# Performance work log

Hardware: AMD Instinct MI355X
Metric: run time of the kernel (lower is better)

The kernel has to match this reference:

```python
import jax, jax.numpy as jnp
import numpy as np

B, D, H = 128, 256, 512  # batch, input_size, hidden_size; 2 hidden layers
ORDER = 'A'
EPS = 1e-12


def _masks():
    # Standard MADE sequential degrees: inputs 1..D (reversed for order 'B'),
    # hidden degrees cycle over 1..D-1. Hidden mask: >=, output mask: > (strict).
    din = np.arange(1, D + 1) if ORDER == 'A' else np.arange(D, 0, -1)
    dh = (np.arange(H) % (D - 1)) + 1
    m0 = (dh[:, None] >= din[None, :]).astype(np.float32)  # [H, D]
    m1 = (dh[:, None] >= dh[None, :]).astype(np.float32)   # [H, H]
    mo = (din[:, None] > dh[None, :]).astype(np.float32)   # [D, H]
    return jnp.asarray(m0), jnp.asarray(m1), jnp.asarray(mo)


def _made(y, W0, b0, W1, b1, Wo, bo, masks):
    m0, m1, mo = masks
    h = jax.nn.elu(y @ (W0 * m0).T + b0)   # [B, H]
    h = jax.nn.elu(h @ (W1 * m1).T + b1)   # [B, H]
    return h @ (Wo * mo).T + bo            # [B, D]


def setup_inputs() -> dict:
    key = jax.random.key(0)
    ks = jax.random.split(key, 13)
    s_in, s_h = 1.0 / np.sqrt(D), 1.0 / np.sqrt(H)

    def p(k, shape, s):
        return (jax.random.normal(k, shape, jnp.float32) * s).astype(jnp.float32)

    return {
        'x': jax.random.normal(ks[0], (B, D), jnp.float32),
        'mu_W0': p(ks[1], (H, D), s_in), 'mu_b0': jnp.zeros((H,), jnp.float32),
        'mu_W1': p(ks[2], (H, H), s_h),  'mu_b1': jnp.zeros((H,), jnp.float32),
        'mu_Wo': p(ks[3], (D, H), s_h),  'mu_bo': jnp.zeros((D,), jnp.float32),
        'lv_W0': p(ks[4], (H, D), s_in), 'lv_b0': jnp.zeros((H,), jnp.float32),
        'lv_W1': p(ks[5], (H, H), s_h),  'lv_b1': jnp.zeros((H,), jnp.float32),
        'lv_Wo': p(ks[6], (D, H), s_h),  'lv_bo': jnp.zeros((D,), jnp.float32),
    }


def reference(x, mu_W0, mu_b0, mu_W1, mu_b1, mu_Wo, mu_bo,
              lv_W0, lv_b0, lv_W1, lv_b1, lv_Wo, lv_bo):
    masks = _masks()
    idx = jnp.arange(D) if ORDER == 'A' else jnp.arange(D - 1, -1, -1)

    def step(carry, i):
        y, _ = carry
        mu = _made(y, mu_W0, mu_b0, mu_W1, mu_b1, mu_Wo, mu_bo, masks)
        logstd = 0.5 * _made(y, lv_W0, lv_b0, lv_W1, lv_b1, lv_Wo, lv_bo, masks)
        new_col = (x[:, i] - mu[:, i]) / (jnp.exp(logstd[:, i]) + EPS)
        y = y.at[:, i].set(new_col)
        return (y, logstd), None

    init = (jnp.zeros_like(x), jnp.zeros_like(x))
    (y, logstd), _ = jax.lax.scan(step, init, idx)
    return y, logstd.sum(axis=1)
```

## Files before the change

### kernel.cpp

```cpp
#include <hip/hip_runtime.h>

#define DD 256
#define HH 512
#define BB 128
#define TS 4096

#define WAITVM(N) asm volatile("s_waitcnt vmcnt(" #N ")" ::: "memory")
#define PIN4(v) asm volatile("" :: "v"((v).x), "v"((v).y), "v"((v).z), "v"((v).w))

__device__ __forceinline__ float elu_f(float x) {
    return x > 0.f ? x : (__expf(x) - 1.f);
}
__device__ __forceinline__ float rlf(float v, int l) {
    return __uint_as_float(__builtin_amdgcn_readlane(__float_as_uint(v), (unsigned)l));
}
__device__ __forceinline__ float f4c(const float4& v, int r) {
    return r == 0 ? v.x : r == 1 ? v.y : r == 2 ? v.z : v.w;
}

__device__ __forceinline__ int pmap(int h) {
    if (h == 510) return 255;
    if (h == 511) return 511;
    return (h < 255) ? (4 * (h & 63) + (h >> 6))
                     : (256 + 4 * ((h - 255) & 63) + ((h - 255) >> 6));
}
__device__ __forceinline__ int p4map(int j) {
    return 4 * (j & 63) + (j >> 6);
}
__device__ __forceinline__ int w1base(int hp) {
    return (hp <= 254) ? hp * TS
         : (hp <= 509) ? (hp - 255) * TS + 1024
         : 255 * TS + ((hp == 510) ? 0 : 1024);
}
__device__ __forceinline__ int wobase(int hp) {
    return (hp <= 254) ? hp * TS + 3072
         : (hp <= 509) ? (hp - 255) * TS + 3584
         : 255 * TS + ((hp == 510) ? 2048 : 2560);
}

__global__ __launch_bounds__(256) void prep(
    const float* __restrict__ w0m_, const float* __restrict__ w0l_,
    const float* __restrict__ w1m_, const float* __restrict__ w1l_,
    const float* __restrict__ wom_, const float* __restrict__ wol_,
    float* __restrict__ tape)
{
    __shared__ float tm[32][33], tl[32][33];
    const int tx = threadIdx.x & 31, ty = threadIdx.x >> 5;
    const unsigned b = blockIdx.x;

    if (b < 256) {
        const int h0 = (int)(b >> 4) << 5, hp0 = (int)(b & 15) << 5;
        #pragma unroll
        for (int j = 0; j < 4; ++j) {
            int r = ty + 8 * j;
            tm[r][tx] = w1m_[(h0 + r) * HH + hp0 + tx];
            tl[r][tx] = w1l_[(h0 + r) * HH + hp0 + tx];
        }
        __syncthreads();
        #pragma unroll
        for (int j = 0; j < 4; ++j) {
            int hp = hp0 + ty + 8 * j;
            int h  = h0 + tx;
            int dh_h = (h <= 254) ? h + 1 : (h <= 509 ? h - 254 : h - 509);
            int dh_p = (hp <= 254) ? hp + 1 : (hp <= 509 ? hp - 254 : hp - 509);
            float mask = (dh_h >= dh_p) ? 1.f : 0.f;
            int base = w1base(hp), p = pmap(h);
            tape[base + p]       = mask * tm[tx][ty + 8 * j];
            tape[base + 512 + p] = mask * tl[tx][ty + 8 * j];
        }
    } else if (b < 384) {
        const int b2 = (int)b - 256;
        const int h0 = (b2 >> 3) << 5, i0 = (b2 & 7) << 5;
        #pragma unroll
        for (int j = 0; j < 4; ++j) {
            int r = ty + 8 * j;
            tm[r][tx] = w0m_[(h0 + r) * DD + i0 + tx];
            tl[r][tx] = w0l_[(h0 + r) * DD + i0 + tx];
        }
        __syncthreads();
        #pragma unroll
        for (int j = 0; j < 4; ++j) {
            int i = i0 + ty + 8 * j;
            int h = h0 + tx;
            int p = pmap(h);
            tape[i * TS + 2048 + p] = tm[tx][ty + 8 * j];
            tape[i * TS + 2560 + p] = tl[tx][ty + 8 * j];
        }
    } else {
        const int b3 = (int)b - 384;
        const int j0 = (b3 >> 4) << 5, hp0 = (b3 & 15) << 5;
        #pragma unroll
        for (int j = 0; j < 4; ++j) {
            int r = ty + 8 * j;
            tm[r][tx] = wom_[(j0 + r) * HH + hp0 + tx];
            tl[r][tx] = wol_[(j0 + r) * HH + hp0 + tx];
        }
        __syncthreads();
        #pragma unroll
        for (int j = 0; j < 4; ++j) {
            int hp = hp0 + ty + 8 * j;
            int jj = j0 + tx;
            int base = wobase(hp), p = p4map(jj);
            tape[base + p]       = tm[tx][ty + 8 * j];
            tape[base + 256 + p] = tl[tx][ty + 8 * j];
        }
    }
}

__device__ __forceinline__ void stage16(const float* g, float* l, int lane) {
    #pragma unroll
    for (int k = 0; k < 16; ++k) {
        __builtin_amdgcn_global_load_lds(
            (const __attribute__((address_space(1))) void*)(g + 256 * k + 4 * lane),
            (__attribute__((address_space(3))) void*)(l + 256 * k),
            16, 0, 0);
    }
}

struct WSet { float4 w[16]; };

__device__ __forceinline__ void rdW(WSet& S, const float* b, int lane) {
    const float4* p = (const float4*)b;
    S.w[8]  = p[64 * 8 + lane];  S.w[9]  = p[64 * 9 + lane];
    S.w[10] = p[64 * 10 + lane]; S.w[11] = p[64 * 11 + lane];
    S.w[0]  = p[64 * 0 + lane];  S.w[4]  = p[64 * 4 + lane];
    S.w[1]  = p[64 * 1 + lane];  S.w[5]  = p[64 * 5 + lane];
    S.w[2]  = p[64 * 2 + lane];  S.w[6]  = p[64 * 6 + lane];
    S.w[3]  = p[64 * 3 + lane];  S.w[7]  = p[64 * 7 + lane];
    S.w[12] = p[64 * 12 + lane]; S.w[14] = p[64 * 14 + lane];
    S.w[13] = p[64 * 13 + lane]; S.w[15] = p[64 * 15 + lane];
}
__device__ __forceinline__ void pinW(const WSet& S) {
    #pragma unroll
    for (int k = 0; k < 16; ++k) PIN4(S.w[k]);
}

template<int Q, int EX>
__device__ __forceinline__ void stepF(
    int tl, int lane, float v, const WSet& S,
    float (&a0m)[8], float (&a0l)[8], float (&a1m)[8], float (&a1l)[8],
    float (&Rm)[4], float (&Rl)[4], float (&yv)[4],
    const float4& exmA, const float4& exmB, const float4& exlA, const float4& exlB,
    const float4& exwm, const float4& exwl)
{
    yv[Q] = (lane == tl) ? v : yv[Q];

    #pragma unroll
    for (int r = Q; r < 4; ++r) {
        a0m[r]     += v * f4c(S.w[8], r);
        a0m[4 + r] += v * f4c(S.w[9], r);
        a0l[r]     += v * f4c(S.w[10], r);
        a0l[4 + r] += v * f4c(S.w[11], r);
    }

    float p0m = elu_f(rlf(a0m[Q], tl)),     p0l = elu_f(rlf(a0l[Q], tl));
    float p1m = elu_f(rlf(a0m[4 + Q], tl)), p1l = elu_f(rlf(a0l[4 + Q], tl));
    float p2m = 0.f, p2l = 0.f;
    if (EX) {
        p2m = elu_f(rlf(a0m[EX == 1 ? 3 : 7], 63));
        p2l = elu_f(rlf(a0l[EX == 1 ? 3 : 7], 63));
    }

    #pragma unroll
    for (int r = Q; r < 4; ++r) {
        a1m[r]     += f4c(S.w[0], r) * p0m + f4c(S.w[4], r) * p1m;
        a1m[4 + r] += f4c(S.w[1], r) * p0m + f4c(S.w[5], r) * p1m;
        a1l[r]     += f4c(S.w[2], r) * p0l + f4c(S.w[6], r) * p1l;
        a1l[4 + r] += f4c(S.w[3], r) * p0l + f4c(S.w[7], r) * p1l;
    }
    if (EX) {
        #pragma unroll
        for (int r = 0; r < 4; ++r) {
            a1m[r]     += f4c(exmA, r) * p2m;
            a1m[4 + r] += f4c(exmB, r) * p2m;
            a1l[r]     += f4c(exlA, r) * p2l;
            a1l[4 + r] += f4c(exlB, r) * p2l;
        }
    }

    float q0m = elu_f(rlf(a1m[Q], tl)),     q0l = elu_f(rlf(a1l[Q], tl));
    float q1m = elu_f(rlf(a1m[4 + Q], tl)), q1l = elu_f(rlf(a1l[4 + Q], tl));
    float q2m = 0.f, q2l = 0.f;
    if (EX) {
        q2m = elu_f(rlf(a1m[EX == 1 ? 3 : 7], 63));
        q2l = elu_f(rlf(a1l[EX == 1 ? 3 : 7], 63));
    }

    #pragma unroll
    for (int r = Q; r < 4; ++r) {
        Rm[r] += f4c(S.w[12], r) * q0m + f4c(S.w[14], r) * q1m;
        Rl[r] += f4c(S.w[13], r) * q0l + f4c(S.w[15], r) * q1l;
    }
    if (EX) {
        #pragma unroll
        for (int r = 0; r < 4; ++r) {
            Rm[r] += f4c(exwm, r) * q2m;
            Rl[r] += f4c(exwl, r) * q2l;
        }
    }
}

__global__ __launch_bounds__(128, 1) void made_main(
    const float* __restrict__ x,
    const float* __restrict__ mu_b0, const float* __restrict__ mu_b1,
    const float* __restrict__ mu_bo,
    const float* __restrict__ lv_b0, const float* __restrict__ lv_b1,
    const float* __restrict__ lv_bo,
    const float* __restrict__ tape,
    float* __restrict__ out)
{
    __shared__ __align__(16) float buf[4][TS];
    const int row  = blockIdx.x;
    const int lane = threadIdx.x & 63;
    const int wid  = threadIdx.x >> 6;

    const float4 d4 = make_float4(0.f, 0.f, 0.f, 0.f);

    if (wid == 1) {
        #pragma unroll
        for (int g = 0; g < 3; ++g)
            stage16(tape + (size_t)g * TS, &buf[g][0], lane);
        #pragma unroll 1
        for (int t = 0; t < 255; ++t) {
            if (t < 253) { WAITVM(16); } else { WAITVM(0); }
            __builtin_amdgcn_s_barrier();
            __builtin_amdgcn_sched_barrier(0);
            int g = t + 3;
            if (g < 255)
                stage16(tape + (size_t)g * TS, &buf[g & 3][0], lane);
        }
        return;
    }

    float a0m[8], a0l[8], a1m[8], a1l[8], Rm[4], Rl[4], yv[4];
    float xv[4], bmv[4], blv[4];
    #pragma unroll
    for (int r = 0; r < 4; ++r) {
        a0m[r]     = mu_b0[lane + 64 * r];
        a0m[4 + r] = mu_b0[255 + lane + 64 * r];
        a0l[r]     = lv_b0[lane + 64 * r];
        a0l[4 + r] = lv_b0[255 + lane + 64 * r];
        a1m[r]     = mu_b1[lane + 64 * r];
        a1m[4 + r] = mu_b1[255 + lane + 64 * r];
        a1l[r]     = lv_b1[lane + 64 * r];
        a1l[4 + r] = lv_b1[255 + lane + 64 * r];
        Rm[r] = 0.f; Rl[r] = 0.f; yv[r] = 0.f;
        xv[r]  = x[row * DD + 64 * r + lane];
        bmv[r] = mu_bo[64 * r + lane];
        blv[r] = lv_bo[64 * r + lane];
    }
    if (lane == 63) {
        a0m[3] = mu_b0[510]; a0m[7] = mu_b0[511];
        a0l[3] = lv_b0[510]; a0l[7] = lv_b0[511];
        a1m[3] = mu_b1[510]; a1m[7] = mu_b1[511];
        a1l[3] = lv_b1[510]; a1l[7] = lv_b1[511];
    }

    const float4* a4 = (const float4*)(tape + 255 * TS);
    float4 e510mA = a4[lane],       e510mB = a4[64 + lane];
    float4 e510lA = a4[128 + lane], e510lB = a4[192 + lane];
    float4 e511mA = a4[256 + lane], e511mB = a4[320 + lane];
    float4 e511lA = a4[384 + lane], e511lB = a4[448 + lane];
    float4 wo510m = a4[512 + lane], wo510l = a4[576 + lane];
    float4 wo511m = a4[640 + lane], wo511l = a4[704 + lane];

    float ls_part = 0.f;
    float vloc;
    {
        float d0  = xv[0] - (Rm[0] + bmv[0]);
        float ls0 = 0.5f * (Rl[0] + blv[0]);
        float s0  = __fdividef(1.f, __expf(ls0) + 1e-12f);
        ls_part += (lane == 0) ? ls0 : 0.f;
        vloc = d0 * s0;
    }

    WSet W;

    __syncthreads();
    rdW(W, &buf[0][0], lane);
    {
        float v = rlf(vloc, 0);
        stepF<0, 1>(0, lane, v, W, a0m, a0l, a1m, a1l, Rm, Rl, yv,
                    e510mA, e510mB, e510lA, e510lB, wo510m, wo510l);
        rdW(W, &buf[1][0], lane);
        float d_  = xv[0] - (Rm[0] + bmv[0]);
        float ls_ = 0.5f * (Rl[0] + blv[0]);
        float s_  = __fdividef(1.f, __expf(ls_) + 1e-12f);
        ls_part += (lane == 1) ? ls_ : 0.f;
        vloc = d_ * s_;
        pinW(W);
    }

    __syncthreads();
    {
        float v = rlf(vloc, 1);
        stepF<0, 2>(1, lane, v, W, a0m, a0l, a1m, a1l, Rm, Rl, yv,
                    e511mA, e511mB, e511lA, e511lB, wo511m, wo511l);
        rdW(W, &buf[2][0], lane);
        float d_  = xv[0] - (Rm[0] + bmv[0]);
        float ls_ = 0.5f * (Rl[0] + blv[0]);
        float s_  = __fdividef(1.f, __expf(ls_) + 1e-12f);
        ls_part += (lane == 2) ? ls_ : 0.f;
        vloc = d_ * s_;
        pinW(W);
    }

#define FBODY(Q, tt, Qn, tn, PREF)                                            \
    {                                                                         \
        __syncthreads();                                                      \
        float v_ = rlf(vloc, (tt) & 63);                                      \
        stepF<Q, 0>((tt) & 63, lane, v_, W, a0m, a0l, a1m, a1l, Rm, Rl, yv,   \
                    d4, d4, d4, d4, d4, d4);                                  \
        if (PREF) rdW(W, &buf[((tt) + 1) & 3][0], lane);                      \
        float dn_  = xv[Qn] - (Rm[Qn] + bmv[Qn]);                             \
        float lsn_ = 0.5f * (Rl[Qn] + blv[Qn]);                               \
        float sn_  = __fdividef(1.f, __expf(lsn_) + 1e-12f);                  \
        ls_part += (lane == (tn)) ? lsn_ : 0.f;                               \
        vloc = dn_ * sn_;                                                     \
        if (PREF) pinW(W);                                                    \
    }

    #pragma unroll 1
    for (int t = 2; t < 63; ++t)    FBODY(0, t, 0, t + 1, 1)
    FBODY(0, 63, 1, 0, 1)
    #pragma unroll 1
    for (int t = 64; t < 127; ++t)  FBODY(1, t, 1, t - 63, 1)
    FBODY(1, 127, 2, 0, 1)
    #pragma unroll 1
    for (int t = 128; t < 191; ++t) FBODY(2, t, 2, t - 127, 1)
    FBODY(2, 191, 3, 0, 1)
    #pragma unroll 1
    for (int t = 192; t < 254; ++t) FBODY(3, t, 3, t - 191, 1)
    FBODY(3, 254, 3, 63, 0)
#undef FBODY

    yv[3] = (lane == 63) ? vloc : yv[3];

    #pragma unroll
    for (int r = 0; r < 4; ++r) out[row * DD + 64 * r + lane] = yv[r];

    #pragma unroll
    for (int off = 32; off; off >>= 1)
        ls_part += __shfl_down(ls_part, off);
    if (lane == 0) out[BB * DD + row] = ls_part;
}

extern "C" void kernel_launch(void* const* d_in, const int* in_sizes, int n_in,
                              void* d_out, int out_size, void* d_ws, size_t ws_size,
                              hipStream_t stream) {
    const float* x     = (const float*)d_in[0];
    const float* mu_W0 = (const float*)d_in[1];
    const float* mu_b0 = (const float*)d_in[2];
    const float* mu_W1 = (const float*)d_in[3];
    const float* mu_b1 = (const float*)d_in[4];
    const float* mu_Wo = (const float*)d_in[5];
    const float* mu_bo = (const float*)d_in[6];
    const float* lv_W0 = (const float*)d_in[7];
    const float* lv_b0 = (const float*)d_in[8];
    const float* lv_W1 = (const float*)d_in[9];
    const float* lv_b1 = (const float*)d_in[10];
    const float* lv_Wo = (const float*)d_in[11];
    const float* lv_bo = (const float*)d_in[12];

    float* tape = (float*)d_ws;

    prep<<<512, 256, 0, stream>>>(mu_W0, lv_W0, mu_W1, lv_W1, mu_Wo, lv_Wo, tape);
    made_main<<<BB, 128, 0, stream>>>(x, mu_b0, mu_b1, mu_bo,
                                      lv_b0, lv_b1, lv_bo, tape, (float*)d_out);
}
```

Measured before the change: 178.4 us.

## Batch tape staging into groups of four steps with an eight-slot LDS ring

The producer wave now stages four tape slices at a time into an 8-deep LDS ring and syncs with the compute wave once per four steps instead of every step. The compute wave drops the software prefetch and register pinning, loading each step's weights from LDS right before use. This is meant to cut per-step barrier overhead. In exchange it doubles LDS use to 128 KB and exposes LDS load latency on each step, since the next step's weights are no longer prefetched.

```diff
diff --git a/kernel.cpp b/kernel.cpp
--- a/kernel.cpp
+++ b/kernel.cpp
@@ -6,7 +6,7 @@
 #define TS 4096
 
 #define WAITVM(N) asm volatile("s_waitcnt vmcnt(" #N ")" ::: "memory")
-#define PIN4(v) asm volatile("" :: "v"((v).x), "v"((v).y), "v"((v).z), "v"((v).w))
+#define SBAR() do { __builtin_amdgcn_s_barrier(); __builtin_amdgcn_sched_barrier(0); } while (0)
 
 __device__ __forceinline__ float elu_f(float x) {
     return x > 0.f ? x : (__expf(x) - 1.f);
@@ -130,10 +130,6 @@
     S.w[12] = p[64 * 12 + lane]; S.w[14] = p[64 * 14 + lane];
     S.w[13] = p[64 * 13 + lane]; S.w[15] = p[64 * 15 + lane];
 }
-__device__ __forceinline__ void pinW(const WSet& S) {
-    #pragma unroll
-    for (int k = 0; k < 16; ++k) PIN4(S.w[k]);
-}
 
 template<int Q, int EX>
 __device__ __forceinline__ void stepF(
@@ -209,7 +205,7 @@
     const float* __restrict__ tape,
     float* __restrict__ out)
 {
-    __shared__ __align__(16) float buf[4][TS];
+    __shared__ __align__(16) float buf[8][TS];
     const int row  = blockIdx.x;
     const int lane = threadIdx.x & 63;
     const int wid  = threadIdx.x >> 6;
@@ -218,16 +214,21 @@
 
     if (wid == 1) {
         #pragma unroll
-        for (int g = 0; g < 3; ++g)
+        for (int g = 0; g < 4; ++g)
             stage16(tape + (size_t)g * TS, &buf[g][0], lane);
+        WAITVM(0);
+        SBAR();
         #pragma unroll 1
-        for (int t = 0; t < 255; ++t) {
-            if (t < 253) { WAITVM(16); } else { WAITVM(0); }
-            __builtin_amdgcn_s_barrier();
-            __builtin_amdgcn_sched_barrier(0);
-            int g = t + 3;
-            if (g < 255)
-                stage16(tape + (size_t)g * TS, &buf[g & 3][0], lane);
+        for (int r = 1; r < 64; ++r) {
+            int base = 4 * r;
+            #pragma unroll
+            for (int k = 0; k < 4; ++k) {
+                int g = base + k;
+                if (g < 255)
+                    stage16(tape + (size_t)g * TS, &buf[g & 7][0], lane);
+            }
+            WAITVM(0);
+            SBAR();
         }
         return;
     }
@@ -276,63 +277,89 @@
 
     WSet W;
 
-    __syncthreads();
-    rdW(W, &buf[0][0], lane);
-    {
-        float v = rlf(vloc, 0);
-        stepF<0, 1>(0, lane, v, W, a0m, a0l, a1m, a1l, Rm, Rl, yv,
-                    e510mA, e510mB, e510lA, e510lB, wo510m, wo510l);
-        rdW(W, &buf[1][0], lane);
-        float d_  = xv[0] - (Rm[0] + bmv[0]);
-        float ls_ = 0.5f * (Rl[0] + blv[0]);
-        float s_  = __fdividef(1.f, __expf(ls_) + 1e-12f);
-        ls_part += (lane == 1) ? ls_ : 0.f;
-        vloc = d_ * s_;
-        pinW(W);
-    }
-
-    __syncthreads();
-    {
-        float v = rlf(vloc, 1);
-        stepF<0, 2>(1, lane, v, W, a0m, a0l, a1m, a1l, Rm, Rl, yv,
-                    e511mA, e511mB, e511lA, e511lB, wo511m, wo511l);
-        rdW(W, &buf[2][0], lane);
-        float d_  = xv[0] - (Rm[0] + bmv[0]);
-        float ls_ = 0.5f * (Rl[0] + blv[0]);
-        float s_  = __fdividef(1.f, __expf(ls_) + 1e-12f);
-        ls_part += (lane == 2) ? ls_ : 0.f;
-        vloc = d_ * s_;
-        pinW(W);
-    }
-
-#define FBODY(Q, tt, Qn, tn, PREF)                                            \
+#define FSTEP(Q, tt, Qn, tn)                                                  \
     {                                                                         \
-        __syncthreads();                                                      \
         float v_ = rlf(vloc, (tt) & 63);                                      \
+        rdW(W, &buf[(tt) & 7][0], lane);                                      \
         stepF<Q, 0>((tt) & 63, lane, v_, W, a0m, a0l, a1m, a1l, Rm, Rl, yv,   \
                     d4, d4, d4, d4, d4, d4);                                  \
-        if (PREF) rdW(W, &buf[((tt) + 1) & 3][0], lane);                      \
         float dn_  = xv[Qn] - (Rm[Qn] + bmv[Qn]);                             \
         float lsn_ = 0.5f * (Rl[Qn] + blv[Qn]);                               \
         float sn_  = __fdividef(1.f, __expf(lsn_) + 1e-12f);                  \
         ls_part += (lane == (tn)) ? lsn_ : 0.f;                               \
         vloc = dn_ * sn_;                                                     \
-        if (PREF) pinW(W);                                                    \
-    }
+    }
+
+    SBAR();
+    {
+        float v0 = rlf(vloc, 0);
+        rdW(W, &buf[0][0], lane);
+        stepF<0, 1>(0, lane, v0, W, a0m, a0l, a1m, a1l, Rm, Rl, yv,
+                    e510mA, e510mB, e510lA, e510lB, wo510m, wo510l);
+        float dn  = xv[0] - (Rm[0] + bmv[0]);
+        float lsn = 0.5f * (Rl[0] + blv[0]);
+        float sn  = __fdividef(1.f, __expf(lsn) + 1e-12f);
+        ls_part += (lane == 1) ? lsn : 0.f;
+        vloc = dn * sn;
+    }
+    {
+        float v1 = rlf(vloc, 1);
+        rdW(W, &buf[1][0], lane);
+        stepF<0, 2>(1, lane, v1, W, a0m, a0l, a1m, a1l, Rm, Rl, yv,
+                    e511mA, e511mB, e511lA, e511lB, wo511m, wo511l);
+        float dn  = xv[0] - (Rm[0] + bmv[0]);
+        float lsn = 0.5f * (Rl[0] + blv[0]);
+        float sn  = __fdividef(1.f, __expf(lsn) + 1e-12f);
+        ls_part += (lane == 2) ? lsn : 0.f;
+        vloc = dn * sn;
+    }
+    FSTEP(0, 2, 0, 3)
+    FSTEP(0, 3, 0, 4)
 
     #pragma unroll 1
-    for (int t = 2; t < 63; ++t)    FBODY(0, t, 0, t + 1, 1)
-    FBODY(0, 63, 1, 0, 1)
+    for (int t = 4; t < 60; t += 4) {
+        SBAR();
+        FSTEP(0, t,     0, t + 1)
+        FSTEP(0, t + 1, 0, t + 2)
+        FSTEP(0, t + 2, 0, t + 3)
+        FSTEP(0, t + 3, 0, t + 4)
+    }
+    SBAR();
+    FSTEP(0, 60, 0, 61) FSTEP(0, 61, 0, 62) FSTEP(0, 62, 0, 63) FSTEP(0, 63, 1, 0)
+
     #pragma unroll 1
-    for (int t = 64; t < 127; ++t)  FBODY(1, t, 1, t - 63, 1)
-    FBODY(1, 127, 2, 0, 1)
+    for (int t = 64; t < 124; t += 4) {
+        SBAR();
+        FSTEP(1, t,     1, t - 63)
+        FSTEP(1, t + 1, 1, t - 62)
+        FSTEP(1, t + 2, 1, t - 61)
+        FSTEP(1, t + 3, 1, t - 60)
+    }
+    SBAR();
+    FSTEP(1, 124, 1, 61) FSTEP(1, 125, 1, 62) FSTEP(1, 126, 1, 63) FSTEP(1, 127, 2, 0)
+
     #pragma unroll 1
-    for (int t = 128; t < 191; ++t) FBODY(2, t, 2, t - 127, 1)
-    FBODY(2, 191, 3, 0, 1)
+    for (int t = 128; t < 188; t += 4) {
+        SBAR();
+        FSTEP(2, t,     2, t - 127)
+        FSTEP(2, t + 1, 2, t - 126)
+        FSTEP(2, t + 2, 2, t - 125)
+        FSTEP(2, t + 3, 2, t - 124)
+    }
+    SBAR();
+    FSTEP(2, 188, 2, 61) FSTEP(2, 189, 2, 62) FSTEP(2, 190, 2, 63) FSTEP(2, 191, 3, 0)
+
     #pragma unroll 1
-    for (int t = 192; t < 254; ++t) FBODY(3, t, 3, t - 191, 1)
-    FBODY(3, 254, 3, 63, 0)
-#undef FBODY
+    for (int t = 192; t < 252; t += 4) {
+        SBAR();
+        FSTEP(3, t,     3, t - 191)
+        FSTEP(3, t + 1, 3, t - 190)
+        FSTEP(3, t + 2, 3, t - 189)
+        FSTEP(3, t + 3, 3, t - 188)
+    }
+    SBAR();
+    FSTEP(3, 252, 3, 61) FSTEP(3, 253, 3, 62) FSTEP(3, 254, 3, 63)
+#undef FSTEP
 
     yv[3] = (lane == 63) ? vloc : yv[3];
 
```

New measurement: 171.6 us. 1.04x faster.
